# Kernel optimization log

Hardware: AMD Instinct MI355X
Metric: run time of the kernel (lower is better)

## Reference

```python
import jax, jax.numpy as jnp
import numpy as np


def setup_inputs() -> dict:
    key = jax.random.key(0)
    k1, k2, k3 = jax.random.split(key, 3)
    B, N, D = 4, 4096, 1024
    x = jax.random.normal(k1, (B, N, D), dtype=jnp.float32)
    # torch nn.Linear default init ~ U(-1/sqrt(D), 1/sqrt(D)); scale normals similarly
    scale = 1.0 / np.sqrt(D)
    Wq = jax.random.normal(k2, (D, D), dtype=jnp.float32) * scale
    Wk = jax.random.normal(k3, (D, D), dtype=jnp.float32) * scale
    return {"x": x, "Wq": Wq, "Wk": Wk}


def reference(x, Wq, Wk):
    # torch Linear: y = x @ W.T (weight shape [out, in])
    D = x.shape[-1]
    q = jnp.einsum('bnd,ed->bne', x, Wq)  # [B,N,D]
    k = jnp.einsum('bnd,ed->bne', x, Wk)  # [B,N,D]
    scores = jnp.einsum('bqd,bkd->bqk', q, k) / jnp.sqrt(jnp.float32(D))
    attn = jax.nn.softmax(scores, axis=-1)  # [B,N,N]
    return jnp.einsum('bqk,bkd->bqd', attn, x)
```

## Files before the change

### kernel.cpp

```cpp
#include <hip/hip_runtime.h>
#include <stdint.h>
#include <math.h>

typedef __attribute__((ext_vector_type(8))) short short8;
typedef __attribute__((ext_vector_type(4))) float fx4;
typedef unsigned int u32;

#define MFMA16(a, b, c) __builtin_amdgcn_mfma_f32_16x16x32_bf16(a, b, c, 0, 0, 0)
#define SCL 0.04508422002777948f

#define CFENCE asm volatile("" ::: "memory")

__device__ __forceinline__ unsigned short f2bfu(float f) {
  unsigned u = __builtin_bit_cast(unsigned, f);
  u += 0x7fffu + ((u >> 16) & 1u);
  return (unsigned short)(u >> 16);
}

__device__ __forceinline__ float fast_exp2(float x) {
  float r;
  asm("v_exp_f32 %0, %1" : "=v"(r) : "v"(x));
  return r;
}

__device__ __forceinline__ void gl_lds16(const void* g, void* l) {
  __builtin_amdgcn_global_load_lds(
      (const __attribute__((address_space(1))) u32*)g,
      (__attribute__((address_space(3))) u32*)l, 16, 0, 0);
}

__device__ __forceinline__ void barx() {
  CFENCE;
  __builtin_amdgcn_s_barrier();
  CFENCE;
}

__global__ __launch_bounds__(256) void prep_kernel(const float* __restrict__ x,
                                                   unsigned short* __restrict__ xT,
                                                   unsigned short* __restrict__ xbf) {
  __shared__ float tile[64 * 65];
  const int b = blockIdx.z, n0 = blockIdx.x * 64, d0 = blockIdx.y * 64;
  const int tid = threadIdx.x;
  const float* xb = x + ((size_t)b * 4096 + n0) * 1024 + d0;
#pragma unroll
  for (int i = 0; i < 4; i++) {
    int idx = tid + 256 * i;
    int r = idx >> 4, c4 = (idx & 15) * 4;
    const float4 v = *(const float4*)(xb + (size_t)r * 1024 + c4);
    float* tp = &tile[r * 65 + c4];
    tp[0] = v.x; tp[1] = v.y; tp[2] = v.z; tp[3] = v.w;
    uint2 pkt;
    pkt.x = (u32)f2bfu(v.x) | ((u32)f2bfu(v.y) << 16);
    pkt.y = (u32)f2bfu(v.z) | ((u32)f2bfu(v.w) << 16);
    *(uint2*)(xbf + ((size_t)b * 4096 + n0 + r) * 1024 + d0 + c4) = pkt;
  }
  __syncthreads();
  unsigned short* xo = xT + ((size_t)b * 1024 + d0) * 4096 + n0;
#pragma unroll
  for (int i = 0; i < 4; i++) {
    int idx = tid + 256 * i;
    int dr = idx >> 4, n4 = (idx & 15) * 4;
    unsigned short h0 = f2bfu(tile[(n4 + 0) * 65 + dr]);
    unsigned short h1 = f2bfu(tile[(n4 + 1) * 65 + dr]);
    unsigned short h2 = f2bfu(tile[(n4 + 2) * 65 + dr]);
    unsigned short h3 = f2bfu(tile[(n4 + 3) * 65 + dr]);
    uint2 pkt;
    pkt.x = (u32)h0 | ((u32)h1 << 16);
    pkt.y = (u32)h2 | ((u32)h3 << 16);
    *(uint2*)(xo + (size_t)dr * 4096 + n4) = pkt;
  }
}

__global__ __launch_bounds__(256) void wconv_kernel(const float* __restrict__ Wq,
                                                    const float* __restrict__ Wk,
                                                    unsigned short* __restrict__ Wqb,
                                                    unsigned short* __restrict__ Wkb) {
  int gid = blockIdx.x * 256 + threadIdx.x;
  const float* s = (gid < 262144) ? Wq : Wk;
  unsigned short* d = (gid < 262144) ? Wqb : Wkb;
  int off = (gid & 262143) * 4;
  const float4 v = *(const float4*)(s + off);
  uint2 pkt;
  pkt.x = (u32)f2bfu(v.x) | ((u32)f2bfu(v.y) << 16);
  pkt.y = (u32)f2bfu(v.z) | ((u32)f2bfu(v.w) << 16);
  *(uint2*)(d + off) = pkt;
}

__device__ __forceinline__ void core256(const unsigned short* __restrict__ Ab,
                                        const unsigned short* __restrict__ Bb,
                                        char* lp, fx4 (&acc)[8][4]) {
  constexpr int NT = 16;
  const int tid = threadIdx.x;
  const int wave = tid >> 6, lane = tid & 63;
  const int wm = wave >> 2, wn = wave & 3;
  const int quad = lane >> 4, l16 = lane & 15;

  const int sr0 = tid >> 3, so0 = (tid & 7) ^ (sr0 & 7);
  const int ga0 = sr0 * 1024 + so0 * 8;
  const int ga1 = ga0 + 64 * 1024;
  const int ld0 = tid * 16;

  const int cst0 = (quad ^ (l16 & 7)) * 16;
  const int cst1 = ((4 + quad) ^ (l16 & 7)) * 16;
  const int arb = wm * 16384 + l16 * 128;
  const int brb = 32768 + (wn >> 1) * 16384 + (wn & 1) * 8192 + l16 * 128;

#pragma unroll
  for (int i = 0; i < 8; i++)
#pragma unroll
    for (int j = 0; j < 4; j++) acc[i][j] = (fx4)0.f;

#define C_STG(OPb, halfb, rowadd, bufb, kte)                                        \
  do {                                                                              \
    gl_lds16(OPb + (size_t)(rowadd) * 1024 + (kte) + ga0, lp + (bufb) + (halfb) + ld0); \
    gl_lds16(OPb + (size_t)(rowadd) * 1024 + (kte) + ga1,                           \
             lp + (bufb) + (halfb) + ld0 + 8192);                                   \
  } while (0)

  C_STG(Bb, 32768, 0, 0, 0);
  C_STG(Ab, 0, 0, 0, 0);
  C_STG(Ab, 16384, 128, 0, 0);
  C_STG(Bb, 49152, 128, 0, 0);
  C_STG(Bb, 32768, 0, 65536, 64);
  C_STG(Ab, 0, 0, 65536, 64);
  asm volatile("s_waitcnt vmcnt(4)" ::: "memory");
  barx();

  short8 af[8], bf0[4], bf1[4];
  for (int t = 0; t < NT; ++t) {
    const int cbo = (t & 1) * 65536, nbo = cbo ^ 65536;
    const int kt1 = ((t + 1) & (NT - 1)) * 64;
    const int kt2 = ((t + 2) & (NT - 1)) * 64;
#pragma unroll
    for (int mt = 0; mt < 4; mt++) {
      af[2 * mt] = *(const short8*)(lp + cbo + arb + mt * 2048 + cst0);
      af[2 * mt + 1] = *(const short8*)(lp + cbo + arb + mt * 2048 + cst1);
    }
#pragma unroll
    for (int nt = 0; nt < 2; nt++) {
      bf0[2 * nt] = *(const short8*)(lp + cbo + brb + nt * 2048 + cst0);
      bf0[2 * nt + 1] = *(const short8*)(lp + cbo + brb + nt * 2048 + cst1);
    }
    C_STG(Ab, 16384, 128, nbo, kt1);
    barx();
    __builtin_amdgcn_s_setprio(1);
#pragma unroll
    for (int mt = 0; mt < 4; mt++)
#pragma unroll
      for (int nt = 0; nt < 2; nt++) {
        acc[mt][nt] = MFMA16(af[2 * mt], bf0[2 * nt], acc[mt][nt]);
        acc[mt][nt] = MFMA16(af[2 * mt + 1], bf0[2 * nt + 1], acc[mt][nt]);
      }
    __builtin_amdgcn_s_setprio(0);
    barx();
#pragma unroll
    for (int nt = 0; nt < 2; nt++) {
      bf1[2 * nt] = *(const short8*)(lp + cbo + brb + (nt + 2) * 2048 + cst0);
      bf1[2 * nt + 1] = *(const short8*)(lp + cbo + brb + (nt + 2) * 2048 + cst1);
    }
    C_STG(Bb, 49152, 128, nbo, kt1);
    barx();
    __builtin_amdgcn_s_setprio(1);
#pragma unroll
    for (int mt = 0; mt < 4; mt++)
#pragma unroll
      for (int nt = 0; nt < 2; nt++) {
        acc[mt][nt + 2] = MFMA16(af[2 * mt], bf1[2 * nt], acc[mt][nt + 2]);
        acc[mt][nt + 2] = MFMA16(af[2 * mt + 1], bf1[2 * nt + 1], acc[mt][nt + 2]);
      }
    __builtin_amdgcn_s_setprio(0);
    barx();
#pragma unroll
    for (int mt = 0; mt < 4; mt++) {
      af[2 * mt] = *(const short8*)(lp + cbo + arb + (mt + 4) * 2048 + cst0);
      af[2 * mt + 1] = *(const short8*)(lp + cbo + arb + (mt + 4) * 2048 + cst1);
    }
    C_STG(Bb, 32768, 0, cbo, kt2);
    barx();
    __builtin_amdgcn_s_setprio(1);
#pragma unroll
    for (int mt = 0; mt < 4; mt++)
#pragma unroll
      for (int nt = 0; nt < 2; nt++) {
        acc[mt + 4][nt + 2] = MFMA16(af[2 * mt], bf1[2 * nt], acc[mt + 4][nt + 2]);
        acc[mt + 4][nt + 2] = MFMA16(af[2 * mt + 1], bf1[2 * nt + 1], acc[mt + 4][nt + 2]);
      }
    __builtin_amdgcn_s_setprio(0);
    barx();
    C_STG(Ab, 0, 0, cbo, kt2);
    asm volatile("s_waitcnt vmcnt(4)" ::: "memory");
    barx();
    __builtin_amdgcn_s_setprio(1);
#pragma unroll
    for (int mt = 0; mt < 4; mt++)
#pragma unroll
      for (int nt = 0; nt < 2; nt++) {
        acc[mt + 4][nt] = MFMA16(af[2 * mt], bf0[2 * nt], acc[mt + 4][nt]);
        acc[mt + 4][nt] = MFMA16(af[2 * mt + 1], bf0[2 * nt + 1], acc[mt + 4][nt]);
      }
    __builtin_amdgcn_s_setprio(0);
    barx();
  }
#undef C_STG
}

template <int ONES, int NT, int LDA, int LDB>
__device__ __forceinline__ void core128(const unsigned short* __restrict__ Ab,
                                        const unsigned short* __restrict__ Bb,
                                        short* lds, fx4 (&acc)[4][4], fx4 (&accl)[4]) {
  constexpr int BUFB = 49152;
  const int tid = threadIdx.x;
  const int wave = tid >> 6, lane = tid & 63;
  const int wm = wave >> 1, wn = wave & 1;
  const int quad = lane >> 4, l16 = lane & 15;
  char* lp = (char*)lds;

  const int sr0 = tid >> 3, so0 = (tid & 7) ^ (sr0 & 7);
  const int ga0 = sr0 * LDA + so0 * 8;
  const int ga1 = ga0 + 64 * LDA;
  const int gb0 = sr0 * LDB + so0 * 8;
  const int ld0 = tid * 16;

  const int cst0 = (quad ^ (l16 & 7)) * 16;
  const int cst1 = ((4 + quad) ^ (l16 & 7)) * 16;
  const int arb = (wm >> 1) * 16384 + (wm & 1) * 8192 + l16 * 128;
  const int brb = 32768 + wn * 8192 + l16 * 128;

  short8 ones;
#pragma unroll
  for (int i = 0; i < 8; i++) ones[i] = (short)0x3F80;
#pragma unroll
  for (int i = 0; i < 4; i++) {
    accl[i] = (fx4)0.f;
#pragma unroll
    for (int j = 0; j < 4; j++) acc[i][j] = (fx4)0.f;
  }

#define PV_STGA(halfb, rowadd, bufb, kte)                                          \
  do {                                                                             \
    gl_lds16(Ab + (size_t)(rowadd) * LDA + (kte) + ga0, lp + (bufb) + (halfb) + ld0); \
    gl_lds16(Ab + (size_t)(rowadd) * LDA + (kte) + ga1,                            \
             lp + (bufb) + (halfb) + ld0 + 8192);                                  \
  } while (0)
#define PV_STGB(halfb, rowadd, bufb, kte) \
  gl_lds16(Bb + (size_t)(rowadd) * LDB + (kte) + gb0, lp + (bufb) + 32768 + (halfb) + ld0)

  PV_STGB(0, 0, 0, 0);
  PV_STGA(0, 0, 0, 0);
  PV_STGA(16384, 128, 0, 0);
  PV_STGB(8192, 64, 0, 0);
  PV_STGB(0, 0, BUFB, 64);
  PV_STGA(0, 0, BUFB, 64);
  asm volatile("s_waitcnt vmcnt(3)" ::: "memory");
  barx();

  short8 af[4], bf0[4], bf1[4];
  for (int t = 0; t < NT; ++t) {
    const int cbo = (t & 1) * BUFB, nbo = cbo ^ BUFB;
    const int kt1 = ((t + 1) & (NT - 1)) * 64;
    const int kt2 = ((t + 2) & (NT - 1)) * 64;
#pragma unroll
    for (int mt = 0; mt < 2; mt++) {
      af[2 * mt] = *(const short8*)(lp + cbo + arb + mt * 2048 + cst0);
      af[2 * mt + 1] = *(const short8*)(lp + cbo + arb + mt * 2048 + cst1);
    }
#pragma unroll
    for (int nt = 0; nt < 2; nt++) {
      bf0[2 * nt] = *(const short8*)(lp + cbo + brb + nt * 2048 + cst0);
      bf0[2 * nt + 1] = *(const short8*)(lp + cbo + brb + nt * 2048 + cst1);
    }
    PV_STGA(16384, 128, nbo, kt1);
    barx();
    __builtin_amdgcn_s_setprio(1);
#pragma unroll
    for (int mt = 0; mt < 2; mt++) {
#pragma unroll
      for (int nt = 0; nt < 2; nt++) {
        acc[mt][nt] = MFMA16(af[2 * mt], bf0[2 * nt], acc[mt][nt]);
        acc[mt][nt] = MFMA16(af[2 * mt + 1], bf0[2 * nt + 1], acc[mt][nt]);
      }
      if (ONES) {
        accl[mt] = MFMA16(af[2 * mt], ones, accl[mt]);
        accl[mt] = MFMA16(af[2 * mt + 1], ones, accl[mt]);
      }
    }
    __builtin_amdgcn_s_setprio(0);
    barx();
#pragma unroll
    for (int nt = 0; nt < 2; nt++) {
      bf1[2 * nt] = *(const short8*)(lp + cbo + brb + (nt + 2) * 2048 + cst0);
      bf1[2 * nt + 1] = *(const short8*)(lp + cbo + brb + (nt + 2) * 2048 + cst1);
    }
    PV_STGB(8192, 64, nbo, kt1);
    barx();
    __builtin_amdgcn_s_setprio(1);
#pragma unroll
    for (int mt = 0; mt < 2; mt++)
#pragma unroll
      for (int nt = 0; nt < 2; nt++) {
        acc[mt][nt + 2] = MFMA16(af[2 * mt], bf1[2 * nt], acc[mt][nt + 2]);
        acc[mt][nt + 2] = MFMA16(af[2 * mt + 1], bf1[2 * nt + 1], acc[mt][nt + 2]);
      }
    __builtin_amdgcn_s_setprio(0);
    barx();
#pragma unroll
    for (int mt = 0; mt < 2; mt++) {
      af[2 * mt] = *(const short8*)(lp + cbo + arb + (mt + 2) * 2048 + cst0);
      af[2 * mt + 1] = *(const short8*)(lp + cbo + arb + (mt + 2) * 2048 + cst1);
    }
    PV_STGB(0, 0, cbo, kt2);
    barx();
    __builtin_amdgcn_s_setprio(1);
#pragma unroll
    for (int mt = 0; mt < 2; mt++) {
#pragma unroll
      for (int nt = 0; nt < 2; nt++) {
        acc[mt + 2][nt + 2] = MFMA16(af[2 * mt], bf1[2 * nt], acc[mt + 2][nt + 2]);
        acc[mt + 2][nt + 2] = MFMA16(af[2 * mt + 1], bf1[2 * nt + 1], acc[mt + 2][nt + 2]);
      }
      if (ONES) {
        accl[mt + 2] = MFMA16(af[2 * mt], ones, accl[mt + 2]);
        accl[mt + 2] = MFMA16(af[2 * mt + 1], ones, accl[mt + 2]);
      }
    }
    __builtin_amdgcn_s_setprio(0);
    barx();
    PV_STGA(0, 0, cbo, kt2);
    asm volatile("s_waitcnt vmcnt(3)" ::: "memory");
    barx();
    __builtin_amdgcn_s_setprio(1);
#pragma unroll
    for (int mt = 0; mt < 2; mt++)
#pragma unroll
      for (int nt = 0; nt < 2; nt++) {
        acc[mt + 2][nt] = MFMA16(af[2 * mt], bf0[2 * nt], acc[mt + 2][nt]);
        acc[mt + 2][nt] = MFMA16(af[2 * mt + 1], bf0[2 * nt + 1], acc[mt + 2][nt]);
      }
    __builtin_amdgcn_s_setprio(0);
    barx();
  }
#undef PV_STGA
#undef PV_STGB
}

__global__ __launch_bounds__(512) void proj_kernel(
    const unsigned short* __restrict__ xbf, const unsigned short* __restrict__ Wqb,
    const unsigned short* __restrict__ Wkb, unsigned short* __restrict__ Qo,
    unsigned short* __restrict__ Ko) {
  __shared__ __attribute__((aligned(16))) short lds[65536];
  const unsigned short* Wb = blockIdx.z ? Wkb : Wqb;
  unsigned short* O = blockIdx.z ? Ko : Qo;
  const int m0 = blockIdx.x * 256, e0 = blockIdx.y * 256;
  fx4 acc[8][4];
  core256(xbf + (size_t)m0 * 1024, Wb + (size_t)e0 * 1024, (char*)lds, acc);
  const int wave = threadIdx.x >> 6, lane = threadIdx.x & 63;
  const int wm = wave >> 2, wn = wave & 3;
  const int quad = lane >> 4, l16 = lane & 15;
#pragma unroll
  for (int mt = 0; mt < 8; mt++) {
    const int row = m0 + wm * 128 + mt * 16 + quad * 4;
#pragma unroll
    for (int nt = 0; nt < 4; nt++) {
      const int col = e0 + wn * 64 + nt * 16 + l16;
      unsigned short* op = O + (size_t)row * 1024 + col;
#pragma unroll
      for (int i = 0; i < 4; i++) op[(size_t)i * 1024] = f2bfu(acc[mt][nt][i]);
    }
  }
}

__global__ __launch_bounds__(512) void qk_kernel(
    const unsigned short* __restrict__ Qb, const unsigned short* __restrict__ Kb,
    unsigned short* __restrict__ Pp, int bbase) {
  __shared__ __attribute__((aligned(16))) short lds[65536];
  const int fid = blockIdx.x + 16 * blockIdx.y + 256 * blockIdx.z;
  const int swz = (fid & 7) * 64 + (fid >> 3);
  const int bx = swz & 15, by = (swz >> 4) & 15, bz = swz >> 8;
  const int b = bbase + bz;
  unsigned short* Pb = Pp + (size_t)bz * 4096 * 4096;
  const int m0 = bx * 256, n0 = by * 256;
  fx4 acc[8][4];
  core256(Qb + (size_t)b * 4096 * 1024 + (size_t)m0 * 1024,
          Kb + (size_t)b * 4096 * 1024 + (size_t)n0 * 1024, (char*)lds, acc);
  const int wave = threadIdx.x >> 6, lane = threadIdx.x & 63;
  const int wm = wave >> 2, wn = wave & 3;
  const int quad = lane >> 4, l16 = lane & 15;
#pragma unroll
  for (int mt = 0; mt < 8; mt++) {
    const int row = m0 + wm * 128 + mt * 16 + quad * 4;
#pragma unroll
    for (int nt = 0; nt < 4; nt++) {
      const int col = n0 + wn * 64 + nt * 16 + l16;
      unsigned short* pp = Pb + (size_t)row * 4096 + col;
#pragma unroll
      for (int i = 0; i < 4; i++)
        pp[(size_t)i * 4096] = f2bfu(fast_exp2(acc[mt][nt][i] * SCL));
    }
  }
}

__global__ __launch_bounds__(512) void pv_kernel(
    const unsigned short* __restrict__ P, const unsigned short* __restrict__ xT,
    unsigned short* __restrict__ Ost, int bbase) {
  __shared__ __attribute__((aligned(16))) short lds[49152];
  const int fid = blockIdx.x + 16 * blockIdx.y + 128 * blockIdx.z;
  const int swz = (fid & 7) * 32 + (fid >> 3);
  const int bx = swz & 15, by = (swz >> 4) & 7, bz = swz >> 7;
  const int b = bbase + bz;
  const int m0 = bx * 256, e0 = by * 128;
  const unsigned short* Ab = P + (size_t)bz * 4096 * 4096 + (size_t)m0 * 4096;
  const unsigned short* Bb = xT + (size_t)b * 1024 * 4096 + (size_t)e0 * 4096;
  fx4 acc[4][4], accl[4];
  core128<1, 64, 4096, 4096>(Ab, Bb, lds, acc, accl);
  unsigned short* O = Ost + (size_t)b * 4096 * 1024;
  const int wave = threadIdx.x >> 6, lane = threadIdx.x & 63;
  const int wm = wave >> 1, wn = wave & 1;
  const int quad = lane >> 4, l16 = lane & 15;
#pragma unroll
  for (int mt = 0; mt < 4; mt++) {
    const int row = m0 + wm * 64 + mt * 16 + quad * 4;
    const fx4 li = accl[mt];
    fx4 r;
#pragma unroll
    for (int i = 0; i < 4; i++) r[i] = __builtin_amdgcn_rcpf(li[i]);
#pragma unroll
    for (int nt = 0; nt < 4; nt++) {
      const int col = e0 + wn * 64 + nt * 16 + l16;
      unsigned short* op = O + (size_t)row * 1024 + col;
#pragma unroll
      for (int i = 0; i < 4; i++) op[(size_t)i * 1024] = f2bfu(acc[mt][nt][i] * r[i]);
    }
  }
}

__global__ __launch_bounds__(256) void fin_kernel(const uint4* __restrict__ Ost,
                                                  float4* __restrict__ out) {
  size_t t = (size_t)blockIdx.x * 256 + threadIdx.x;
  const uint4 v = Ost[t];
  float4 o0, o1;
  o0.x = __builtin_bit_cast(float, v.x << 16);
  o0.y = __builtin_bit_cast(float, v.x & 0xffff0000u);
  o0.z = __builtin_bit_cast(float, v.y << 16);
  o0.w = __builtin_bit_cast(float, v.y & 0xffff0000u);
  o1.x = __builtin_bit_cast(float, v.z << 16);
  o1.y = __builtin_bit_cast(float, v.z & 0xffff0000u);
  o1.z = __builtin_bit_cast(float, v.w << 16);
  o1.w = __builtin_bit_cast(float, v.w & 0xffff0000u);
  out[t * 2] = o0;
  out[t * 2 + 1] = o1;
}

extern "C" void kernel_launch(void* const* d_in, const int* in_sizes, int n_in,
                              void* d_out, int out_size, void* d_ws, size_t ws_size,
                              hipStream_t stream) {
  const float* x = (const float*)d_in[0];
  const float* Wq = (const float*)d_in[1];
  const float* Wk = (const float*)d_in[2];
  char* ws = (char*)d_ws;
  unsigned short* xT = (unsigned short*)ws;
  unsigned short* Qb = (unsigned short*)(ws + (size_t)33554432);
  unsigned short* Kb = (unsigned short*)(ws + (size_t)67108864);
  unsigned short* Ost = Qb;
  unsigned short* xbf = (unsigned short*)d_out;
  unsigned short* Wqb = (unsigned short*)((char*)d_out + (size_t)33554432);
  unsigned short* Wkb = (unsigned short*)((char*)d_out + (size_t)35651584);
  unsigned short* Pp = (unsigned short*)d_out;

  hipLaunchKernelGGL(prep_kernel, dim3(64, 16, 4), dim3(256), 0, stream, x, xT, xbf);
  hipLaunchKernelGGL(wconv_kernel, dim3(2048), dim3(256), 0, stream, Wq, Wk, Wqb, Wkb);
  hipLaunchKernelGGL(proj_kernel, dim3(64, 4, 2), dim3(512), 0, stream, xbf, Wqb, Wkb, Qb, Kb);
  hipLaunchKernelGGL(qk_kernel, dim3(16, 16, 2), dim3(512), 0, stream, Qb, Kb, Pp, 0);
  hipLaunchKernelGGL(pv_kernel, dim3(16, 8, 2), dim3(512), 0, stream, Pp, xT, Ost, 0);
  hipLaunchKernelGGL(qk_kernel, dim3(16, 16, 2), dim3(512), 0, stream, Qb, Kb, Pp, 2);
  hipLaunchKernelGGL(pv_kernel, dim3(16, 8, 2), dim3(512), 0, stream, Pp, xT, Ost, 2);
  hipLaunchKernelGGL(fin_kernel, dim3(8192), dim3(256), 0, stream,
                     (const uint4*)Ost, (float4*)d_out);
}
```

Measured before the change: 468.6 us.

## Compute softmax row sums in QK epilogue via atomics, drop in-PV rowsum MFMA

The QK kernel now accumulates per-row sums of the exponentiated scores in fp32, reduces them across lanes with shuffles, and atomically adds them into a workspace buffer that the weight-conversion kernel zeroes. The PV kernel reads these sums for normalisation and instantiates core128 with the extra row-sum accumulation disabled, removing that work from the PV inner loop. The block-index swizzle for L2 locality is also removed from both kernels, which may change cache reuse. The new path adds atomics and shuffles in the QK epilogue and is used only when the workspace is large enough.

```diff
diff --git a/kernel.cpp b/kernel.cpp
--- a/kernel.cpp
+++ b/kernel.cpp
@@ -74,8 +74,10 @@
 __global__ __launch_bounds__(256) void wconv_kernel(const float* __restrict__ Wq,
                                                     const float* __restrict__ Wk,
                                                     unsigned short* __restrict__ Wqb,
-                                                    unsigned short* __restrict__ Wkb) {
+                                                    unsigned short* __restrict__ Wkb,
+                                                    float* __restrict__ rsum) {
   int gid = blockIdx.x * 256 + threadIdx.x;
+  if (rsum && gid < 16384) rsum[gid] = 0.f;
   const float* s = (gid < 262144) ? Wq : Wk;
   unsigned short* d = (gid < 262144) ? Wqb : Wkb;
   int off = (gid & 262143) * 4;
@@ -369,22 +371,27 @@
   }
 }
 
+template <int RS>
 __global__ __launch_bounds__(512) void qk_kernel(
     const unsigned short* __restrict__ Qb, const unsigned short* __restrict__ Kb,
-    unsigned short* __restrict__ Pp, int bbase) {
+    unsigned short* __restrict__ Pp, float* __restrict__ rsum, int bbase) {
   __shared__ __attribute__((aligned(16))) short lds[65536];
-  const int fid = blockIdx.x + 16 * blockIdx.y + 256 * blockIdx.z;
-  const int swz = (fid & 7) * 64 + (fid >> 3);
-  const int bx = swz & 15, by = (swz >> 4) & 15, bz = swz >> 8;
-  const int b = bbase + bz;
+  const int bz = blockIdx.z, b = bbase + bz;
   unsigned short* Pb = Pp + (size_t)bz * 4096 * 4096;
-  const int m0 = bx * 256, n0 = by * 256;
+  const int m0 = blockIdx.x * 256, n0 = blockIdx.y * 256;
   fx4 acc[8][4];
   core256(Qb + (size_t)b * 4096 * 1024 + (size_t)m0 * 1024,
           Kb + (size_t)b * 4096 * 1024 + (size_t)n0 * 1024, (char*)lds, acc);
   const int wave = threadIdx.x >> 6, lane = threadIdx.x & 63;
   const int wm = wave >> 2, wn = wave & 3;
   const int quad = lane >> 4, l16 = lane & 15;
+  float sums[8][4];
+  if (RS) {
+#pragma unroll
+    for (int mt = 0; mt < 8; mt++)
+#pragma unroll
+      for (int i = 0; i < 4; i++) sums[mt][i] = 0.f;
+  }
 #pragma unroll
   for (int mt = 0; mt < 8; mt++) {
     const int row = m0 + wm * 128 + mt * 16 + quad * 4;
@@ -393,33 +400,53 @@
       const int col = n0 + wn * 64 + nt * 16 + l16;
       unsigned short* pp = Pb + (size_t)row * 4096 + col;
 #pragma unroll
-      for (int i = 0; i < 4; i++)
-        pp[(size_t)i * 4096] = f2bfu(fast_exp2(acc[mt][nt][i] * SCL));
-    }
-  }
-}
-
+      for (int i = 0; i < 4; i++) {
+        float pe = fast_exp2(acc[mt][nt][i] * SCL);
+        pp[(size_t)i * 4096] = f2bfu(pe);
+        if (RS) sums[mt][i] += pe;
+      }
+    }
+  }
+  if (RS) {
+    float* rb = rsum + (size_t)b * 4096 + m0 + wm * 128;
+#pragma unroll
+    for (int mt = 0; mt < 8; mt++)
+#pragma unroll
+      for (int i = 0; i < 4; i++) {
+        float s = sums[mt][i];
+        s += __shfl_xor(s, 1);
+        s += __shfl_xor(s, 2);
+        s += __shfl_xor(s, 4);
+        s += __shfl_xor(s, 8);
+        if (l16 == 0) atomicAdd(rb + mt * 16 + quad * 4 + i, s);
+      }
+  }
+}
+
+template <int RS>
 __global__ __launch_bounds__(512) void pv_kernel(
     const unsigned short* __restrict__ P, const unsigned short* __restrict__ xT,
-    unsigned short* __restrict__ Ost, int bbase) {
+    const float* __restrict__ rsum, unsigned short* __restrict__ Ost, int bbase) {
   __shared__ __attribute__((aligned(16))) short lds[49152];
-  const int fid = blockIdx.x + 16 * blockIdx.y + 128 * blockIdx.z;
-  const int swz = (fid & 7) * 32 + (fid >> 3);
-  const int bx = swz & 15, by = (swz >> 4) & 7, bz = swz >> 7;
-  const int b = bbase + bz;
-  const int m0 = bx * 256, e0 = by * 128;
+  const int bz = blockIdx.z, b = bbase + bz;
+  const int m0 = blockIdx.x * 256, e0 = blockIdx.y * 128;
   const unsigned short* Ab = P + (size_t)bz * 4096 * 4096 + (size_t)m0 * 4096;
   const unsigned short* Bb = xT + (size_t)b * 1024 * 4096 + (size_t)e0 * 4096;
   fx4 acc[4][4], accl[4];
-  core128<1, 64, 4096, 4096>(Ab, Bb, lds, acc, accl);
+  core128<RS ? 0 : 1, 64, 4096, 4096>(Ab, Bb, lds, acc, accl);
   unsigned short* O = Ost + (size_t)b * 4096 * 1024;
   const int wave = threadIdx.x >> 6, lane = threadIdx.x & 63;
   const int wm = wave >> 1, wn = wave & 1;
   const int quad = lane >> 4, l16 = lane & 15;
+  const float* rb = RS ? (rsum + (size_t)b * 4096 + m0 + wm * 64) : nullptr;
 #pragma unroll
   for (int mt = 0; mt < 4; mt++) {
     const int row = m0 + wm * 64 + mt * 16 + quad * 4;
-    const fx4 li = accl[mt];
+    fx4 li;
+    if (RS)
+      li = *(const fx4*)(rb + mt * 16 + quad * 4);
+    else
+      li = accl[mt];
     fx4 r;
 #pragma unroll
     for (int i = 0; i < 4; i++) r[i] = __builtin_amdgcn_rcpf(li[i]);
@@ -466,13 +493,23 @@
   unsigned short* Wkb = (unsigned short*)((char*)d_out + (size_t)35651584);
   unsigned short* Pp = (unsigned short*)d_out;
 
+  const bool rs = ws_size >= (size_t)100663296 + 65536;
+  float* rsum = rs ? (float*)(ws + (size_t)100663296) : nullptr;
+
   hipLaunchKernelGGL(prep_kernel, dim3(64, 16, 4), dim3(256), 0, stream, x, xT, xbf);
-  hipLaunchKernelGGL(wconv_kernel, dim3(2048), dim3(256), 0, stream, Wq, Wk, Wqb, Wkb);
+  hipLaunchKernelGGL(wconv_kernel, dim3(2048), dim3(256), 0, stream, Wq, Wk, Wqb, Wkb, rsum);
   hipLaunchKernelGGL(proj_kernel, dim3(64, 4, 2), dim3(512), 0, stream, xbf, Wqb, Wkb, Qb, Kb);
-  hipLaunchKernelGGL(qk_kernel, dim3(16, 16, 2), dim3(512), 0, stream, Qb, Kb, Pp, 0);
-  hipLaunchKernelGGL(pv_kernel, dim3(16, 8, 2), dim3(512), 0, stream, Pp, xT, Ost, 0);
-  hipLaunchKernelGGL(qk_kernel, dim3(16, 16, 2), dim3(512), 0, stream, Qb, Kb, Pp, 2);
-  hipLaunchKernelGGL(pv_kernel, dim3(16, 8, 2), dim3(512), 0, stream, Pp, xT, Ost, 2);
+  if (rs) {
+    hipLaunchKernelGGL((qk_kernel<1>), dim3(16, 16, 2), dim3(512), 0, stream, Qb, Kb, Pp, rsum, 0);
+    hipLaunchKernelGGL((pv_kernel<1>), dim3(16, 8, 2), dim3(512), 0, stream, Pp, xT, rsum, Ost, 0);
+    hipLaunchKernelGGL((qk_kernel<1>), dim3(16, 16, 2), dim3(512), 0, stream, Qb, Kb, Pp, rsum, 2);
+    hipLaunchKernelGGL((pv_kernel<1>), dim3(16, 8, 2), dim3(512), 0, stream, Pp, xT, rsum, Ost, 2);
+  } else {
+    hipLaunchKernelGGL((qk_kernel<0>), dim3(16, 16, 2), dim3(512), 0, stream, Qb, Kb, Pp, rsum, 0);
+    hipLaunchKernelGGL((pv_kernel<0>), dim3(16, 8, 2), dim3(512), 0, stream, Pp, xT, rsum, Ost, 0);
+    hipLaunchKernelGGL((qk_kernel<0>), dim3(16, 16, 2), dim3(512), 0, stream, Qb, Kb, Pp, rsum, 2);
+    hipLaunchKernelGGL((pv_kernel<0>), dim3(16, 8, 2), dim3(512), 0, stream, Pp, xT, rsum, Ost, 2);
+  }
   hipLaunchKernelGGL(fin_kernel, dim3(8192), dim3(256), 0, stream,
                      (const uint4*)Ost, (float4*)d_out);
 }
```

New measurement: 513.4 us. +9.6%, slower.
